# Performance work log

Measured on AMD Instinct MI355X. Metric: run time of the kernel, lower is better.

## Reference

```python
import jax, jax.numpy as jnp
import numpy as np

EPS = 1e-7
ROUTING_ITERS = 3

def squash(s, axis=-1):
    # v = (|s|^2 / (1+|s|^2)) * s / |s|
    sq = jnp.sum(jnp.square(s), axis=axis, keepdims=True)
    return (sq / (1.0 + sq)) * s / jnp.sqrt(sq + EPS)

def setup_inputs() -> dict:
    key = jax.random.key(0)
    k1, k2 = jax.random.split(key)
    B, NI, DI = 64, 2048, 8      # batch, input capsules, input capsule dim
    NC, DC = 32, 16              # output capsules, output capsule dim
    x = jax.random.normal(k1, (B, NI, DI), dtype=jnp.float32)
    W = jax.random.normal(k2, (NC, NI, DC, DI), dtype=jnp.float32) * 0.05
    return {"x": x, "W": W}

def reference(x, W):
    # x: [B, NI, DI], W: [NC, NI, DC, DI]
    # tf.einsum('iabc,abdc->iabd') == project each input capsule per output capsule
    u = jnp.einsum('bif,cidf->bcid', x, W)          # [B, NC, NI, DC]
    B, NC, NI, DC = u.shape
    b = jnp.zeros((B, NC, NI, 1), dtype=u.dtype)
    v = None
    for _ in range(ROUTING_ITERS):
        c = jax.nn.softmax(b, axis=1)                # coupling over output capsules
        s = jnp.sum(c * u, axis=2, keepdims=True)    # [B, NC, 1, DC]
        v = squash(s, axis=-1)                       # [B, NC, 1, DC]
        # original: reduce_sum(matmul(u, tile(v)^T), axis=3) == NI * <u_i, v>
        agree = jnp.sum(u * v, axis=-1, keepdims=True)  # [B, NC, NI, 1]
        b = b + NI * agree
    return jnp.squeeze(v, axis=2)                    # [B, NC, DC]
```

## Files before the change

### kernel.cpp

```cpp
#include <hip/hip_runtime.h>

#define NI 2048
#define NB 64
#define NC 32
#define DC 16
#define DI 8

static constexpr float SQ_EPS = 1e-7f;

typedef float f8 __attribute__((ext_vector_type(8)));

template <int MODE>
__global__
__attribute__((amdgpu_flat_work_group_size(256, 256), amdgpu_waves_per_eu(2, 2)))
void route_pass(
    const float* __restrict__ x, const float* __restrict__ W,
    const float* __restrict__ veff, float* __restrict__ partial)
{
    __shared__ float4 wbuf[4224];
    __shared__ float4 xbuf[128];

    const int tid   = threadIdx.x;
    const int wave  = tid >> 6;
    const int lane  = tid & 63;
    const int c     = lane & 31;
    const int dg    = lane >> 5;
    const int brel0 = wave * 4;
    const int b0    = blockIdx.y * 16 + brel0;

    f8 s0 = {}, s1 = {}, s2 = {}, s3 = {};

    f8 va = {}, vb = {}, vc = {}, vd = {};
    if (MODE == 1) {
        va = *reinterpret_cast<const f8*>(veff + (((size_t)(b0+0)*2 + dg)*32 + c)*8);
        vb = *reinterpret_cast<const f8*>(veff + (((size_t)(b0+1)*2 + dg)*32 + c)*8);
        vc = *reinterpret_cast<const f8*>(veff + (((size_t)(b0+2)*2 + dg)*32 + c)*8);
        vd = *reinterpret_cast<const f8*>(veff + (((size_t)(b0+3)*2 + dg)*32 + c)*8);
    }

    for (int oct = 0; oct < 4; ++oct) {
        const int i0 = blockIdx.x * 16 + oct * 4;
        __syncthreads();
        {
            const int k  = tid & 31;
            const int p0 = tid >> 5;
            const int k10 = k & 15, kdg = k >> 4;
            for (int r = 0; r < 16; ++r) {
                const int p  = r * 8 + p0;
                const int cc = p >> 2;
                const int il = p & 3;
                wbuf[((il * 16 + k10) * 2 + kdg) * 33 + cc] =
                    reinterpret_cast<const float4*>(W)[
                        ((size_t)cc * NI + i0 + il) * 32 + k];
            }
        }
        if (tid < 128) {
            const int k    = tid & 7;
            const int brel = tid >> 3;
            xbuf[brel * 8 + k] = reinterpret_cast<const float4*>(x)[
                ((size_t)(blockIdx.y * 16 + brel) * NI + i0) * 2 + k];
        }
        __syncthreads();

        for (int il = 0; il < 4; ++il) {
            const float4 xa0 = xbuf[(brel0+0)*8 + il*2], xa1 = xbuf[(brel0+0)*8 + il*2+1];
            const float4 xb0 = xbuf[(brel0+1)*8 + il*2], xb1 = xbuf[(brel0+1)*8 + il*2+1];
            const float4 xc0 = xbuf[(brel0+2)*8 + il*2], xc1 = xbuf[(brel0+2)*8 + il*2+1];
            const float4 xd0 = xbuf[(brel0+3)*8 + il*2], xd1 = xbuf[(brel0+3)*8 + il*2+1];

            f8 u0 = {}, u1 = {}, u2 = {}, u3 = {};
#pragma unroll
            for (int dd = 0; dd < 8; ++dd) {
                const float4 wl = wbuf[((il*16 + dd*2    )*2 + dg)*33 + c];
                const float4 wh = wbuf[((il*16 + dd*2 + 1)*2 + dg)*33 + c];
                u0[dd] = wl.x*xa0.x + wl.y*xa0.y + wl.z*xa0.z + wl.w*xa0.w
                       + wh.x*xa1.x + wh.y*xa1.y + wh.z*xa1.z + wh.w*xa1.w;
                u1[dd] = wl.x*xb0.x + wl.y*xb0.y + wl.z*xb0.z + wl.w*xb0.w
                       + wh.x*xb1.x + wh.y*xb1.y + wh.z*xb1.z + wh.w*xb1.w;
                u2[dd] = wl.x*xc0.x + wl.y*xc0.y + wl.z*xc0.z + wl.w*xc0.w
                       + wh.x*xc1.x + wh.y*xc1.y + wh.z*xc1.z + wh.w*xc1.w;
                u3[dd] = wl.x*xd0.x + wl.y*xd0.y + wl.z*xd0.z + wl.w*xd0.w
                       + wh.x*xd1.x + wh.y*xd1.y + wh.z*xd1.z + wh.w*xd1.w;
            }

            if (MODE == 0) {
                const float cu = 1.0f / 32.0f;
                s0 += u0 * cu; s1 += u1 * cu; s2 += u2 * cu; s3 += u3 * cu;
            } else {
#pragma unroll
                for (int pr = 0; pr < 2; ++pr) {
                    const f8& ue = pr ? u2 : u0;
                    const f8& uo = pr ? u3 : u1;
                    const f8& ve = pr ? vc : va;
                    const f8& vo = pr ? vd : vb;
                    float pe = 0.0f, po = 0.0f;
#pragma unroll
                    for (int k = 0; k < 8; ++k) {
                        pe += ue[k] * ve[k];
                        po += uo[k] * vo[k];
                    }
                    const float send = (dg == 0) ? po : pe;
                    const float recv = __shfl_xor(send, 32);
                    float a = ((dg == 0) ? pe : po) + recv;
                    float m = a;
#pragma unroll
                    for (int off = 16; off >= 1; off >>= 1)
                        m = fmaxf(m, __shfl_xor(m, off));
                    const float e = __expf(a - m);
                    float t = e;
#pragma unroll
                    for (int off = 16; off >= 1; off >>= 1)
                        t += __shfl_xor(t, off);
                    const float mine  = e / t;
                    const float other = __shfl_xor(mine, 32);
                    const float ce = (dg == 0) ? mine : other;
                    const float co = (dg == 0) ? other : mine;
                    if (pr == 0) { s0 += u0 * ce; s1 += u1 * co; }
                    else         { s2 += u2 * ce; s3 += u3 * co; }
                }
            }
        }
    }

    {
        const int pblk = blockIdx.y * gridDim.x + blockIdx.x;
        float* gp = partial +
            (((size_t)pblk * 16 + brel0) * 128 + dg * 64 + c * 2) * 4;
        *reinterpret_cast<f8*>(gp)        = s0;
        *reinterpret_cast<f8*>(gp +  512) = s1;
        *reinterpret_cast<f8*>(gp + 1024) = s2;
        *reinterpret_cast<f8*>(gp + 1536) = s3;
    }
}

__global__ __launch_bounds__(128) void reduce_squash(
    const float* __restrict__ partial, float* __restrict__ veff,
    float* __restrict__ out, int phase)
{
    const int b  = blockIdx.x;
    const int c  = (threadIdx.x >> 2) & 31;
    const int dq = threadIdx.x & 3;

    const float* base = partial
        + ((size_t)(b >> 4) * 2048 + (b & 15)) * 512
        + (dq >> 1) * 256 + c * 8 + (dq & 1) * 4;
    float4 acc = make_float4(0.f, 0.f, 0.f, 0.f);
#pragma unroll 8
    for (int ib = 0; ib < 128; ++ib) {
        const float4 p = *reinterpret_cast<const float4*>(base + (size_t)ib * 8192);
        acc.x += p.x; acc.y += p.y; acc.z += p.z; acc.w += p.w;
    }

    float sq = acc.x*acc.x + acc.y*acc.y + acc.z*acc.z + acc.w*acc.w;
    sq += __shfl_xor(sq, 1);
    sq += __shfl_xor(sq, 2);
    const float scale = sq / ((1.0f + sq) * sqrtf(sq + SQ_EPS));

    if (phase == 3) {
        float4* op = reinterpret_cast<float4*>(out + ((size_t)b * NC + c) * DC + dq * 4);
        *op = make_float4(scale*acc.x, scale*acc.y, scale*acc.z, scale*acc.w);
    } else {
        const float ns = scale * (float)NI;
        float4* vp = reinterpret_cast<float4*>(
            veff + (((size_t)b * 2 + (dq >> 1)) * 32 + c) * 8 + (dq & 1) * 4);
        if (phase == 1) {
            *vp = make_float4(ns*acc.x, ns*acc.y, ns*acc.z, ns*acc.w);
        } else {
            float4 old = *vp;
            *vp = make_float4(old.x + ns*acc.x, old.y + ns*acc.y,
                              old.z + ns*acc.z, old.w + ns*acc.w);
        }
    }
}

extern "C" void kernel_launch(void* const* d_in, const int* in_sizes, int n_in,
                              void* d_out, int out_size, void* d_ws, size_t ws_size,
                              hipStream_t stream) {
    (void)in_sizes; (void)n_in; (void)out_size; (void)ws_size;
    const float* x = (const float*)d_in[0];
    const float* W = (const float*)d_in[1];

    float* partial = (float*)d_ws;
    float* veff    = (float*)d_out;

    const dim3 grid(128, 4);

    route_pass<0><<<grid, 256, 0, stream>>>(x, W, nullptr, partial);
    reduce_squash<<<64, 128, 0, stream>>>(partial, veff, nullptr, 1);

    route_pass<1><<<grid, 256, 0, stream>>>(x, W, veff, partial);
    reduce_squash<<<64, 128, 0, stream>>>(partial, veff, nullptr, 2);

    route_pass<1><<<grid, 256, 0, stream>>>(x, W, veff, partial);
    reduce_squash<<<64, 128, 0, stream>>>(partial, nullptr, (float*)d_out, 3);
}
```

Baseline: 200.5 us.

## Split input-capsule range across two wave groups and parallelize partial reduction

The routing kernel now uses 512 threads per block. Two groups of four waves each process half of the block's 16 input capsules, and their per-batch sums are combined through shared memory before being written out. The x tile for all 16 capsules is loaded once up front, and W is staged in four rounds of two capsules per half. The reduce kernel splits its 128-partial sum across four thread groups and combines them in shared memory. The intent is more waves in flight to hide latency, at the cost of an extra LDS combine step and barrier.

```diff
diff --git a/kernel.cpp b/kernel.cpp
--- a/kernel.cpp
+++ b/kernel.cpp
@@ -10,23 +10,28 @@
 
 typedef float f8 __attribute__((ext_vector_type(8)));
 
+union F8u { f8 v; float4 q[2]; };
+
 template <int MODE>
 __global__
-__attribute__((amdgpu_flat_work_group_size(256, 256), amdgpu_waves_per_eu(2, 2)))
+__attribute__((amdgpu_flat_work_group_size(512, 512), amdgpu_waves_per_eu(4)))
 void route_pass(
     const float* __restrict__ x, const float* __restrict__ W,
     const float* __restrict__ veff, float* __restrict__ partial)
 {
     __shared__ float4 wbuf[4224];
-    __shared__ float4 xbuf[128];
+    __shared__ float4 xbuf[512];
 
     const int tid   = threadIdx.x;
     const int wave  = tid >> 6;
     const int lane  = tid & 63;
     const int c     = lane & 31;
     const int dg    = lane >> 5;
-    const int brel0 = wave * 4;
+    const int bq    = wave & 3;
+    const int ih    = wave >> 2;
+    const int brel0 = bq * 4;
     const int b0    = blockIdx.y * 16 + brel0;
+    const int i0    = blockIdx.x * 16;
 
     f8 s0 = {}, s1 = {}, s2 = {}, s3 = {};
 
@@ -38,41 +43,46 @@
         vd = *reinterpret_cast<const f8*>(veff + (((size_t)(b0+3)*2 + dg)*32 + c)*8);
     }
 
-    for (int oct = 0; oct < 4; ++oct) {
-        const int i0 = blockIdx.x * 16 + oct * 4;
+    {
+        const int brel = tid >> 5;
+        const int q    = tid & 31;
+        xbuf[tid] = reinterpret_cast<const float4*>(x)[
+            ((size_t)(blockIdx.y * 16 + brel) * NI + i0) * 2 + q];
+    }
+
+    for (int rnd = 0; rnd < 4; ++rnd) {
         __syncthreads();
         {
-            const int k  = tid & 31;
-            const int p0 = tid >> 5;
+            const int k    = tid & 31;
+            const int rowp = tid >> 5;
             const int k10 = k & 15, kdg = k >> 4;
-            for (int r = 0; r < 16; ++r) {
-                const int p  = r * 8 + p0;
-                const int cc = p >> 2;
-                const int il = p & 3;
-                wbuf[((il * 16 + k10) * 2 + kdg) * 33 + cc] =
+#pragma unroll
+            for (int r = 0; r < 8; ++r) {
+                const int row = r * 16 + rowp;
+                const int cc  = row >> 2;
+                const int sub = row & 3;
+                wbuf[((sub * 16 + k10) * 2 + kdg) * 33 + cc] =
                     reinterpret_cast<const float4*>(W)[
-                        ((size_t)cc * NI + i0 + il) * 32 + k];
-            }
-        }
-        if (tid < 128) {
-            const int k    = tid & 7;
-            const int brel = tid >> 3;
-            xbuf[brel * 8 + k] = reinterpret_cast<const float4*>(x)[
-                ((size_t)(blockIdx.y * 16 + brel) * NI + i0) * 2 + k];
+                        ((size_t)cc * NI + i0 + (sub >> 1) * 8 + rnd * 2
+                         + (sub & 1)) * 32 + k];
+            }
         }
         __syncthreads();
 
-        for (int il = 0; il < 4; ++il) {
-            const float4 xa0 = xbuf[(brel0+0)*8 + il*2], xa1 = xbuf[(brel0+0)*8 + il*2+1];
-            const float4 xb0 = xbuf[(brel0+1)*8 + il*2], xb1 = xbuf[(brel0+1)*8 + il*2+1];
-            const float4 xc0 = xbuf[(brel0+2)*8 + il*2], xc1 = xbuf[(brel0+2)*8 + il*2+1];
-            const float4 xd0 = xbuf[(brel0+3)*8 + il*2], xd1 = xbuf[(brel0+3)*8 + il*2+1];
+#pragma unroll
+        for (int il = 0; il < 2; ++il) {
+            const int slot = ih * 2 + il;
+            const int iloc = ih * 8 + rnd * 2 + il;
+            const float4 xa0 = xbuf[(brel0+0)*32 + iloc*2], xa1 = xbuf[(brel0+0)*32 + iloc*2+1];
+            const float4 xb0 = xbuf[(brel0+1)*32 + iloc*2], xb1 = xbuf[(brel0+1)*32 + iloc*2+1];
+            const float4 xc0 = xbuf[(brel0+2)*32 + iloc*2], xc1 = xbuf[(brel0+2)*32 + iloc*2+1];
+            const float4 xd0 = xbuf[(brel0+3)*32 + iloc*2], xd1 = xbuf[(brel0+3)*32 + iloc*2+1];
 
             f8 u0 = {}, u1 = {}, u2 = {}, u3 = {};
 #pragma unroll
             for (int dd = 0; dd < 8; ++dd) {
-                const float4 wl = wbuf[((il*16 + dd*2    )*2 + dg)*33 + c];
-                const float4 wh = wbuf[((il*16 + dd*2 + 1)*2 + dg)*33 + c];
+                const float4 wl = wbuf[((slot*16 + dd*2    )*2 + dg)*33 + c];
+                const float4 wh = wbuf[((slot*16 + dd*2 + 1)*2 + dg)*33 + c];
                 u0[dd] = wl.x*xa0.x + wl.y*xa0.y + wl.z*xa0.z + wl.w*xa0.w
                        + wh.x*xa1.x + wh.y*xa1.y + wh.z*xa1.z + wh.w*xa1.w;
                 u1[dd] = wl.x*xb0.x + wl.y*xb0.y + wl.z*xb0.z + wl.w*xb0.w
@@ -122,7 +132,23 @@
         }
     }
 
-    {
+    __syncthreads();
+    const int mbase = (brel0 * 64 + lane) * 2;
+    if (ih == 1) {
+        F8u t;
+        t.v = s0; wbuf[mbase      ] = t.q[0]; wbuf[mbase +   1] = t.q[1];
+        t.v = s1; wbuf[mbase + 128] = t.q[0]; wbuf[mbase + 129] = t.q[1];
+        t.v = s2; wbuf[mbase + 256] = t.q[0]; wbuf[mbase + 257] = t.q[1];
+        t.v = s3; wbuf[mbase + 384] = t.q[0]; wbuf[mbase + 385] = t.q[1];
+    }
+    __syncthreads();
+    if (ih == 0) {
+        F8u t;
+        t.q[0] = wbuf[mbase      ]; t.q[1] = wbuf[mbase +   1]; s0 += t.v;
+        t.q[0] = wbuf[mbase + 128]; t.q[1] = wbuf[mbase + 129]; s1 += t.v;
+        t.q[0] = wbuf[mbase + 256]; t.q[1] = wbuf[mbase + 257]; s2 += t.v;
+        t.q[0] = wbuf[mbase + 384]; t.q[1] = wbuf[mbase + 385]; s3 += t.v;
+
         const int pblk = blockIdx.y * gridDim.x + blockIdx.x;
         float* gp = partial +
             (((size_t)pblk * 16 + brel0) * 128 + dg * 64 + c * 2) * 4;
@@ -133,42 +159,57 @@
     }
 }
 
-__global__ __launch_bounds__(128) void reduce_squash(
+__global__ __launch_bounds__(512) void reduce_squash(
     const float* __restrict__ partial, float* __restrict__ veff,
     float* __restrict__ out, int phase)
 {
-    const int b  = blockIdx.x;
-    const int c  = (threadIdx.x >> 2) & 31;
-    const int dq = threadIdx.x & 3;
+    __shared__ float4 red[512];
+    const int b   = blockIdx.x;
+    const int sub = threadIdx.x & 127;
+    const int ibq = threadIdx.x >> 7;
+    const int c   = (sub >> 2) & 31;
+    const int dq  = sub & 3;
 
     const float* base = partial
         + ((size_t)(b >> 4) * 2048 + (b & 15)) * 512
-        + (dq >> 1) * 256 + c * 8 + (dq & 1) * 4;
+        + (dq >> 1) * 256 + c * 8 + (dq & 1) * 4
+        + (size_t)ibq * 32 * 8192;
     float4 acc = make_float4(0.f, 0.f, 0.f, 0.f);
 #pragma unroll 8
-    for (int ib = 0; ib < 128; ++ib) {
+    for (int ib = 0; ib < 32; ++ib) {
         const float4 p = *reinterpret_cast<const float4*>(base + (size_t)ib * 8192);
         acc.x += p.x; acc.y += p.y; acc.z += p.z; acc.w += p.w;
     }
-
-    float sq = acc.x*acc.x + acc.y*acc.y + acc.z*acc.z + acc.w*acc.w;
-    sq += __shfl_xor(sq, 1);
-    sq += __shfl_xor(sq, 2);
-    const float scale = sq / ((1.0f + sq) * sqrtf(sq + SQ_EPS));
-
-    if (phase == 3) {
-        float4* op = reinterpret_cast<float4*>(out + ((size_t)b * NC + c) * DC + dq * 4);
-        *op = make_float4(scale*acc.x, scale*acc.y, scale*acc.z, scale*acc.w);
-    } else {
-        const float ns = scale * (float)NI;
-        float4* vp = reinterpret_cast<float4*>(
-            veff + (((size_t)b * 2 + (dq >> 1)) * 32 + c) * 8 + (dq & 1) * 4);
-        if (phase == 1) {
-            *vp = make_float4(ns*acc.x, ns*acc.y, ns*acc.z, ns*acc.w);
+    red[threadIdx.x] = acc;
+    __syncthreads();
+    if (threadIdx.x < 128) {
+        const float4 a1 = red[sub + 128];
+        const float4 a2 = red[sub + 256];
+        const float4 a3 = red[sub + 384];
+        acc.x += a1.x + a2.x + a3.x;
+        acc.y += a1.y + a2.y + a3.y;
+        acc.z += a1.z + a2.z + a3.z;
+        acc.w += a1.w + a2.w + a3.w;
+
+        float sq = acc.x*acc.x + acc.y*acc.y + acc.z*acc.z + acc.w*acc.w;
+        sq += __shfl_xor(sq, 1);
+        sq += __shfl_xor(sq, 2);
+        const float scale = sq / ((1.0f + sq) * sqrtf(sq + SQ_EPS));
+
+        if (phase == 3) {
+            float4* op = reinterpret_cast<float4*>(out + ((size_t)b * NC + c) * DC + dq * 4);
+            *op = make_float4(scale*acc.x, scale*acc.y, scale*acc.z, scale*acc.w);
         } else {
-            float4 old = *vp;
-            *vp = make_float4(old.x + ns*acc.x, old.y + ns*acc.y,
-                              old.z + ns*acc.z, old.w + ns*acc.w);
+            const float ns = scale * (float)NI;
+            float4* vp = reinterpret_cast<float4*>(
+                veff + (((size_t)b * 2 + (dq >> 1)) * 32 + c) * 8 + (dq & 1) * 4);
+            if (phase == 1) {
+                *vp = make_float4(ns*acc.x, ns*acc.y, ns*acc.z, ns*acc.w);
+            } else {
+                float4 old = *vp;
+                *vp = make_float4(old.x + ns*acc.x, old.y + ns*acc.y,
+                                  old.z + ns*acc.z, old.w + ns*acc.w);
+            }
         }
     }
 }
@@ -185,12 +226,12 @@
 
     const dim3 grid(128, 4);
 
-    route_pass<0><<<grid, 256, 0, stream>>>(x, W, nullptr, partial);
-    reduce_squash<<<64, 128, 0, stream>>>(partial, veff, nullptr, 1);
-
-    route_pass<1><<<grid, 256, 0, stream>>>(x, W, veff, partial);
-    reduce_squash<<<64, 128, 0, stream>>>(partial, veff, nullptr, 2);
-
-    route_pass<1><<<grid, 256, 0, stream>>>(x, W, veff, partial);
-    reduce_squash<<<64, 128, 0, stream>>>(partial, nullptr, (float*)d_out, 3);
+    route_pass<0><<<grid, 512, 0, stream>>>(x, W, nullptr, partial);
+    reduce_squash<<<64, 512, 0, stream>>>(partial, veff, nullptr, 1);
+
+    route_pass<1><<<grid, 512, 0, stream>>>(x, W, veff, partial);
+    reduce_squash<<<64, 512, 0, stream>>>(partial, veff, nullptr, 2);
+
+    route_pass<1><<<grid, 512, 0, stream>>>(x, W, veff, partial);
+    reduce_squash<<<64, 512, 0, stream>>>(partial, nullptr, (float*)d_out, 3);
 }
```

Measured after the change: 344.2 us. +71.7%, slower.
